# Kernel optimization log

Measured on AMD Instinct MI355X. Metric: run time of the kernel, lower is better.

Reference implementation:

```python
import jax, jax.numpy as jnp
import numpy as np

N = 1024
D_IN = 512
D = 128
E = 8192


def setup_inputs() -> dict:
    key = jax.random.key(0)
    ks = jax.random.split(key, 7)
    return {
        "inputs": jax.random.normal(ks[0], (N, D_IN), dtype=jnp.float32),
        "adj": jax.random.uniform(ks[1], (N, N), dtype=jnp.float32),
        "weight": jax.random.normal(ks[2], (D_IN, D), dtype=jnp.float32) * 0.05,
        "weight_two": jax.random.normal(ks[3], (2 * D, D), dtype=jnp.float32) * 0.05,
        "weight_three": jax.random.normal(ks[4], (2 * D, 1), dtype=jnp.float32) * 0.05,
        "train_edges": jax.random.randint(ks[5], (E, 2), 0, N, dtype=jnp.int64 if jax.config.jax_enable_x64 else jnp.int32),
        "train_false_edges": jax.random.randint(ks[6], (E, 2), 0, N, dtype=jnp.int64 if jax.config.jax_enable_x64 else jnp.int32),
    }


def reference(inputs, adj, weight, weight_two, weight_three, train_edges, train_false_edges):
    # encoder: x = X W ; z = A x   (single GCN-style layer, no bias)
    x = inputs @ weight          # (N, D)
    z = adj @ x                  # (N, D)
    n, d = z.shape

    # all-pairs features: pair (i, j) -> [z_i ; z_j]  (torch repeat/reshape semantics)
    z1 = jnp.broadcast_to(z[:, None, :], (n, n, d))   # z1[i,j] = z[i]
    z2 = jnp.broadcast_to(z[None, :, :], (n, n, d))   # z2[i,j] = z[j]

    z_pair = jax.nn.relu(jnp.concatenate([z1, z2], axis=-1))   # (N, N, 2D)
    z_pair = jnp.einsum('ijk,kl->ijl', z_pair, weight_two)     # (N, N, D)
    z_em = z1 * z2                                             # (N, N, D)

    score = jnp.einsum('ijk,kl->ijl', jnp.concatenate([z_pair, z_em], axis=-1), weight_three)
    return jax.nn.sigmoid(score[..., 0])  # (N, N)
```

## Files before the change

### kernel.cpp

```cpp
#include <hip/hip_runtime.h>
#include <math.h>

#define NN 1024
#define DIN 512
#define DD 128

static constexpr long S = (long)NN * DD;
static constexpr long XP_OFF = 0;
static constexpr long ZP_OFF = XP_OFF + 16 * S;
static constexpr long X_OFF  = ZP_OFF + 16 * S;
static constexpr long Z_OFF  = X_OFF + S;
static constexpr long U_OFF  = Z_OFF + S;
static constexpr long A_OFF  = U_OFF + 256;
static constexpr long B_OFF  = A_OFF + NN;

__global__ __launch_bounds__(256) void gemm_part(
    const float* __restrict__ A, const float* __restrict__ B,
    float* __restrict__ Cp, int K, int Kc) {
  const int t = threadIdx.x;
  const int tx = t & 31;
  const int ty = t >> 5;
  const int row0 = blockIdx.x * 32;
  const int k0 = blockIdx.y * Kc;

  float acc[4][4] = {};

  for (int k = k0; k < k0 + Kc; k += 4) {
    float bv[4][4];
#pragma unroll
    for (int kk = 0; kk < 4; ++kk) {
      const float* Brow = &B[(long)(k + kk) * DD + tx];
#pragma unroll
      for (int mc = 0; mc < 4; ++mc) bv[kk][mc] = Brow[32 * mc];
    }
#pragma unroll
    for (int mr = 0; mr < 4; ++mr) {
      const int r = row0 + ty + 8 * mr;
      const float4 av = *(const float4*)&A[(long)r * K + k];
      const float ar[4] = {av.x, av.y, av.z, av.w};
#pragma unroll
      for (int kk = 0; kk < 4; ++kk)
#pragma unroll
        for (int mc = 0; mc < 4; ++mc) acc[mr][mc] += ar[kk] * bv[kk][mc];
    }
  }

  float* Cs = Cp + (long)blockIdx.y * S;
#pragma unroll
  for (int mr = 0; mr < 4; ++mr) {
    const int r = row0 + ty + 8 * mr;
#pragma unroll
    for (int mc = 0; mc < 4; ++mc)
      Cs[(long)r * DD + tx + 32 * mc] = acc[mr][mc];
  }
}

__global__ __launch_bounds__(256) void reduce_x_u(
    const float* __restrict__ xp, float* __restrict__ x,
    const float* __restrict__ W2, const float* __restrict__ w3,
    float* __restrict__ u) {
  const long i = (long)blockIdx.x * 256 + threadIdx.x;
  float s = 0.f;
#pragma unroll
  for (int p = 0; p < 16; ++p) s += xp[p * S + i];
  x[i] = s;

  if (blockIdx.x == 0) {
    const int kq = threadIdx.x;
    float uu = 0.f;
#pragma unroll 4
    for (int l = 0; l < DD; ++l) uu += W2[(long)kq * DD + l] * w3[l];
    u[kq] = uu;
  }
}

__global__ __launch_bounds__(128) void finalize_z(
    const float* __restrict__ zp, float* __restrict__ z,
    const float* __restrict__ u, float* __restrict__ a, float* __restrict__ b) {
  __shared__ float red[2][2];
  const int i = blockIdx.x;
  const int c = threadIdx.x;
  float s = 0.f;
#pragma unroll
  for (int p = 0; p < 16; ++p) s += zp[p * S + (long)i * DD + c];
  z[(long)i * DD + c] = s;

  const float r = s > 0.f ? s : 0.f;
  float pa = r * u[c];
  float pb = r * u[DD + c];
#pragma unroll
  for (int off = 32; off > 0; off >>= 1) {
    pa += __shfl_down(pa, off);
    pb += __shfl_down(pb, off);
  }
  const int w = c >> 6;
  if ((c & 63) == 0) { red[w][0] = pa; red[w][1] = pb; }
  __syncthreads();
  if (c == 0) {
    a[i] = red[0][0] + red[1][0];
    b[i] = red[0][1] + red[1][1];
  }
}

__global__ __launch_bounds__(256) void k4_decode(
    const float* __restrict__ z, const float* __restrict__ w3,
    const float* __restrict__ a, const float* __restrict__ b,
    float* __restrict__ out) {
  __shared__ float zwl[64 * DD];
  const int t = threadIdx.x;
  const int i0 = blockIdx.y * 64;
  const int j0 = blockIdx.x * 64;

#pragma unroll
  for (int s = 0; s < 8; ++s) {
    const int q = s * 256 + t;
    const int r = q >> 5;
    const int k4 = (q & 31) << 2;
    float4 w = *(const float4*)&z[(long)(j0 + r) * DD + k4];
    const float4 cc = *(const float4*)&w3[DD + k4];
    w.x *= cc.x; w.y *= cc.y; w.z *= cc.z; w.w *= cc.w;
    *(float4*)&zwl[r * DD + (k4 ^ ((r & 7) << 2))] = w;
  }
  __syncthreads();

  const int tx = t & 15;
  const int ty = t >> 4;
  float acc[4][4] = {};
  for (int k4 = 0; k4 < DD; k4 += 4) {
    float4 ar[4], bc[4];
#pragma unroll
    for (int m = 0; m < 4; ++m)
      ar[m] = *(const float4*)&z[(long)(i0 + ty + 16 * m) * DD + k4];
#pragma unroll
    for (int m = 0; m < 4; ++m) {
      const int C = tx + 16 * m;
      bc[m] = *(const float4*)&zwl[C * DD + (k4 ^ ((C & 7) << 2))];
    }
#pragma unroll
    for (int mr = 0; mr < 4; ++mr)
#pragma unroll
      for (int mc = 0; mc < 4; ++mc)
        acc[mr][mc] += ar[mr].x * bc[mc].x + ar[mr].y * bc[mc].y +
                       ar[mr].z * bc[mc].z + ar[mr].w * bc[mc].w;
  }

#pragma unroll
  for (int mr = 0; mr < 4; ++mr) {
    const int i = i0 + ty + 16 * mr;
    const float ai = a[i];
#pragma unroll
    for (int mc = 0; mc < 4; ++mc) {
      const int j = j0 + tx + 16 * mc;
      const float sc = ai + b[j] + acc[mr][mc];
      out[(long)i * NN + j] = 1.0f / (1.0f + __expf(-sc));
    }
  }
}

extern "C" void kernel_launch(void* const* d_in, const int* in_sizes, int n_in,
                              void* d_out, int out_size, void* d_ws, size_t ws_size,
                              hipStream_t stream) {
  (void)in_sizes; (void)n_in; (void)out_size; (void)ws_size;
  const float* inputs = (const float*)d_in[0];
  const float* adj    = (const float*)d_in[1];
  const float* weight = (const float*)d_in[2];
  const float* W2     = (const float*)d_in[3];
  const float* w3     = (const float*)d_in[4];
  float* out = (float*)d_out;

  float* ws = (float*)d_ws;
  float* xp = ws + XP_OFF;
  float* zp = ws + ZP_OFF;
  float* x  = ws + X_OFF;
  float* z  = ws + Z_OFF;
  float* u  = ws + U_OFF;
  float* a  = ws + A_OFF;
  float* b  = ws + B_OFF;

  gemm_part<<<dim3(32, 16), 256, 0, stream>>>(inputs, weight, xp, DIN, DIN / 16);
  reduce_x_u<<<512, 256, 0, stream>>>(xp, x, W2, w3, u);
  gemm_part<<<dim3(32, 16), 256, 0, stream>>>(adj, x, zp, NN, NN / 16);
  finalize_z<<<1024, 128, 0, stream>>>(zp, z, u, a, b);
  k4_decode<<<dim3(16, 16), 256, 0, stream>>>(z, w3, a, b, out);
}
```

Baseline: 109.6 us.

## Fuse all stages into one cooperative kernel with grid-wide syncs

Replaces the five separate kernel launches with a single cooperative kernel of 256 blocks that runs every stage in sequence, separated by grid.sync(). The K split of both GEMMs drops from 16 to 8 so the 256-block grid covers them, and the per-stage reductions are remapped to that block count. The aim is to remove per-launch overhead and inter-kernel gaps. In exchange, each GEMM stage now runs with half as many blocks and twice the K-chunk per block, and the grid barriers carry their own cost.

```diff
diff --git a/kernel.cpp b/kernel.cpp
--- a/kernel.cpp
+++ b/kernel.cpp
@@ -1,27 +1,30 @@
 #include <hip/hip_runtime.h>
+#include <hip/hip_cooperative_groups.h>
 #include <math.h>
+
+namespace cg = cooperative_groups;
 
 #define NN 1024
 #define DIN 512
 #define DD 128
+#define NSPLIT 8
 
 static constexpr long S = (long)NN * DD;
 static constexpr long XP_OFF = 0;
-static constexpr long ZP_OFF = XP_OFF + 16 * S;
-static constexpr long X_OFF  = ZP_OFF + 16 * S;
+static constexpr long ZP_OFF = XP_OFF + NSPLIT * S;
+static constexpr long X_OFF  = ZP_OFF + NSPLIT * S;
 static constexpr long Z_OFF  = X_OFF + S;
 static constexpr long U_OFF  = Z_OFF + S;
 static constexpr long A_OFF  = U_OFF + 256;
 static constexpr long B_OFF  = A_OFF + NN;
 
-__global__ __launch_bounds__(256) void gemm_part(
+__device__ __forceinline__ void gemm_part_dev(
     const float* __restrict__ A, const float* __restrict__ B,
-    float* __restrict__ Cp, int K, int Kc) {
-  const int t = threadIdx.x;
+    float* __restrict__ Cp, int K, int Kc, int bid, int t) {
   const int tx = t & 31;
   const int ty = t >> 5;
-  const int row0 = blockIdx.x * 32;
-  const int k0 = blockIdx.y * Kc;
+  const int row0 = (bid & 31) * 32;
+  const int k0 = (bid >> 5) * Kc;
 
   float acc[4][4] = {};
 
@@ -45,7 +48,7 @@
     }
   }
 
-  float* Cs = Cp + (long)blockIdx.y * S;
+  float* Cs = Cp + (long)(bid >> 5) * S;
 #pragma unroll
   for (int mr = 0; mr < 4; ++mr) {
     const int r = row0 + ty + 8 * mr;
@@ -55,104 +58,125 @@
   }
 }
 
-__global__ __launch_bounds__(256) void reduce_x_u(
-    const float* __restrict__ xp, float* __restrict__ x,
-    const float* __restrict__ W2, const float* __restrict__ w3,
-    float* __restrict__ u) {
-  const long i = (long)blockIdx.x * 256 + threadIdx.x;
-  float s = 0.f;
-#pragma unroll
-  for (int p = 0; p < 16; ++p) s += xp[p * S + i];
-  x[i] = s;
-
-  if (blockIdx.x == 0) {
-    const int kq = threadIdx.x;
-    float uu = 0.f;
-#pragma unroll 4
-    for (int l = 0; l < DD; ++l) uu += W2[(long)kq * DD + l] * w3[l];
-    u[kq] = uu;
-  }
-}
-
-__global__ __launch_bounds__(128) void finalize_z(
-    const float* __restrict__ zp, float* __restrict__ z,
-    const float* __restrict__ u, float* __restrict__ a, float* __restrict__ b) {
-  __shared__ float red[2][2];
-  const int i = blockIdx.x;
-  const int c = threadIdx.x;
-  float s = 0.f;
-#pragma unroll
-  for (int p = 0; p < 16; ++p) s += zp[p * S + (long)i * DD + c];
-  z[(long)i * DD + c] = s;
-
-  const float r = s > 0.f ? s : 0.f;
-  float pa = r * u[c];
-  float pb = r * u[DD + c];
-#pragma unroll
-  for (int off = 32; off > 0; off >>= 1) {
-    pa += __shfl_down(pa, off);
-    pb += __shfl_down(pb, off);
-  }
-  const int w = c >> 6;
-  if ((c & 63) == 0) { red[w][0] = pa; red[w][1] = pb; }
-  __syncthreads();
-  if (c == 0) {
-    a[i] = red[0][0] + red[1][0];
-    b[i] = red[0][1] + red[1][1];
-  }
-}
-
-__global__ __launch_bounds__(256) void k4_decode(
-    const float* __restrict__ z, const float* __restrict__ w3,
-    const float* __restrict__ a, const float* __restrict__ b,
-    float* __restrict__ out) {
+__global__ __launch_bounds__(256) void fused(
+    const float* __restrict__ inputs, const float* __restrict__ adj,
+    const float* __restrict__ weight, const float* __restrict__ W2,
+    const float* __restrict__ w3, float* __restrict__ out,
+    float* __restrict__ ws) {
+  cg::grid_group grid = cg::this_grid();
   __shared__ float zwl[64 * DD];
+
   const int t = threadIdx.x;
-  const int i0 = blockIdx.y * 64;
-  const int j0 = blockIdx.x * 64;
-
-#pragma unroll
-  for (int s = 0; s < 8; ++s) {
-    const int q = s * 256 + t;
-    const int r = q >> 5;
-    const int k4 = (q & 31) << 2;
-    float4 w = *(const float4*)&z[(long)(j0 + r) * DD + k4];
-    const float4 cc = *(const float4*)&w3[DD + k4];
-    w.x *= cc.x; w.y *= cc.y; w.z *= cc.z; w.w *= cc.w;
-    *(float4*)&zwl[r * DD + (k4 ^ ((r & 7) << 2))] = w;
-  }
-  __syncthreads();
-
-  const int tx = t & 15;
-  const int ty = t >> 4;
-  float acc[4][4] = {};
-  for (int k4 = 0; k4 < DD; k4 += 4) {
-    float4 ar[4], bc[4];
-#pragma unroll
-    for (int m = 0; m < 4; ++m)
-      ar[m] = *(const float4*)&z[(long)(i0 + ty + 16 * m) * DD + k4];
-#pragma unroll
-    for (int m = 0; m < 4; ++m) {
-      const int C = tx + 16 * m;
-      bc[m] = *(const float4*)&zwl[C * DD + (k4 ^ ((C & 7) << 2))];
-    }
-#pragma unroll
-    for (int mr = 0; mr < 4; ++mr)
-#pragma unroll
-      for (int mc = 0; mc < 4; ++mc)
-        acc[mr][mc] += ar[mr].x * bc[mc].x + ar[mr].y * bc[mc].y +
-                       ar[mr].z * bc[mc].z + ar[mr].w * bc[mc].w;
-  }
-
-#pragma unroll
-  for (int mr = 0; mr < 4; ++mr) {
-    const int i = i0 + ty + 16 * mr;
-    const float ai = a[i];
-#pragma unroll
-    for (int mc = 0; mc < 4; ++mc) {
-      const int j = j0 + tx + 16 * mc;
-      const float sc = ai + b[j] + acc[mr][mc];
-      out[(long)i * NN + j] = 1.0f / (1.0f + __expf(-sc));
+  const int bid = blockIdx.x;
+
+  float* xp = ws + XP_OFF;
+  float* zp = ws + ZP_OFF;
+  float* x  = ws + X_OFF;
+  float* z  = ws + Z_OFF;
+  float* u  = ws + U_OFF;
+  float* a  = ws + A_OFF;
+  float* b  = ws + B_OFF;
+
+  gemm_part_dev(inputs, weight, xp, DIN, DIN / NSPLIT, bid, t);
+  grid.sync();
+
+  {
+    const long i0 = (long)bid * 512;
+    float s0 = 0.f, s1 = 0.f;
+#pragma unroll
+    for (int p = 0; p < NSPLIT; ++p) {
+      s0 += xp[p * S + i0 + t];
+      s1 += xp[p * S + i0 + 256 + t];
+    }
+    x[i0 + t] = s0;
+    x[i0 + 256 + t] = s1;
+
+    if (t < 64) {
+      float p = W2[(long)bid * DD + t] * w3[t] +
+                W2[(long)bid * DD + 64 + t] * w3[64 + t];
+#pragma unroll
+      for (int off = 32; off > 0; off >>= 1) p += __shfl_down(p, off);
+      if (t == 0) u[bid] = p;
+    }
+  }
+  grid.sync();
+
+  gemm_part_dev(adj, x, zp, NN, NN / NSPLIT, bid, t);
+  grid.sync();
+
+  {
+    const int w = t >> 6;
+    const int l = t & 63;
+    const int i = 4 * bid + w;
+    const long base = (long)i * DD + 2 * l;
+    float s0 = 0.f, s1 = 0.f;
+#pragma unroll
+    for (int p = 0; p < NSPLIT; ++p) {
+      const float2 v = *(const float2*)&zp[p * S + base];
+      s0 += v.x; s1 += v.y;
+    }
+    *(float2*)&z[base] = make_float2(s0, s1);
+
+    const float r0 = s0 > 0.f ? s0 : 0.f;
+    const float r1 = s1 > 0.f ? s1 : 0.f;
+    float pa = r0 * u[2 * l] + r1 * u[2 * l + 1];
+    float pb = r0 * u[DD + 2 * l] + r1 * u[DD + 2 * l + 1];
+#pragma unroll
+    for (int off = 32; off > 0; off >>= 1) {
+      pa += __shfl_down(pa, off);
+      pb += __shfl_down(pb, off);
+    }
+    if (l == 0) { a[i] = pa; b[i] = pb; }
+  }
+  grid.sync();
+
+  {
+    const int i0 = (bid >> 4) * 64;
+    const int j0 = (bid & 15) * 64;
+
+#pragma unroll
+    for (int s = 0; s < 8; ++s) {
+      const int q = s * 256 + t;
+      const int r = q >> 5;
+      const int k4 = (q & 31) << 2;
+      float4 wv = *(const float4*)&z[(long)(j0 + r) * DD + k4];
+      const float4 cc = *(const float4*)&w3[DD + k4];
+      wv.x *= cc.x; wv.y *= cc.y; wv.z *= cc.z; wv.w *= cc.w;
+      *(float4*)&zwl[r * DD + (k4 ^ ((r & 7) << 2))] = wv;
+    }
+    __syncthreads();
+
+    const int tx = t & 15;
+    const int ty = t >> 4;
+    float acc[4][4] = {};
+    for (int k4 = 0; k4 < DD; k4 += 4) {
+      float4 ar[4], bc[4];
+#pragma unroll
+      for (int m = 0; m < 4; ++m)
+        ar[m] = *(const float4*)&z[(long)(i0 + ty + 16 * m) * DD + k4];
+#pragma unroll
+      for (int m = 0; m < 4; ++m) {
+        const int C = tx + 16 * m;
+        bc[m] = *(const float4*)&zwl[C * DD + (k4 ^ ((C & 7) << 2))];
+      }
+#pragma unroll
+      for (int mr = 0; mr < 4; ++mr)
+#pragma unroll
+        for (int mc = 0; mc < 4; ++mc)
+          acc[mr][mc] += ar[mr].x * bc[mc].x + ar[mr].y * bc[mc].y +
+                         ar[mr].z * bc[mc].z + ar[mr].w * bc[mc].w;
+    }
+
+#pragma unroll
+    for (int mr = 0; mr < 4; ++mr) {
+      const int i = i0 + ty + 16 * mr;
+      const float ai = a[i];
+#pragma unroll
+      for (int mc = 0; mc < 4; ++mc) {
+        const int j = j0 + tx + 16 * mc;
+        const float sc = ai + b[j] + acc[mr][mc];
+        out[(long)i * NN + j] = 1.0f / (1.0f + __expf(-sc));
+      }
     }
   }
 }
@@ -167,19 +191,10 @@
   const float* W2     = (const float*)d_in[3];
   const float* w3     = (const float*)d_in[4];
   float* out = (float*)d_out;
-
-  float* ws = (float*)d_ws;
-  float* xp = ws + XP_OFF;
-  float* zp = ws + ZP_OFF;
-  float* x  = ws + X_OFF;
-  float* z  = ws + Z_OFF;
-  float* u  = ws + U_OFF;
-  float* a  = ws + A_OFF;
-  float* b  = ws + B_OFF;
-
-  gemm_part<<<dim3(32, 16), 256, 0, stream>>>(inputs, weight, xp, DIN, DIN / 16);
-  reduce_x_u<<<512, 256, 0, stream>>>(xp, x, W2, w3, u);
-  gemm_part<<<dim3(32, 16), 256, 0, stream>>>(adj, x, zp, NN, NN / 16);
-  finalize_z<<<1024, 128, 0, stream>>>(zp, z, u, a, b);
-  k4_decode<<<dim3(16, 16), 256, 0, stream>>>(z, w3, a, b, out);
+  float* ws  = (float*)d_ws;
+
+  void* args[] = {(void*)&inputs, (void*)&adj, (void*)&weight, (void*)&W2,
+                  (void*)&w3, (void*)&out, (void*)&ws};
+  hipLaunchCooperativeKernel((const void*)fused, dim3(256), dim3(256), args,
+                             0, stream);
 }
```

Result: slower. 236.5 us (+115.7%).

## Retile GEMMs to 16-row blocks with 8-way K split and vectorized loads

Applied to the files above, without the earlier changes.

The split-K GEMMs now use 16-row tiles with float4 loads and stores of B and C, and the K split drops from 16 to 8 partials, which shrinks the partial-sum buffers and the reduction reads. The W2·w3 vector product moves out of the reduce kernel into an extra grid row of the first GEMM, so it runs alongside that GEMM. The decode kernel uses 32-row output tiles, which doubles its block count to 512 for better CU coverage. Each thread now does less arithmetic per load, so the per-block work and reuse are lower.

```diff
diff --git a/kernel.cpp b/kernel.cpp
--- a/kernel.cpp
+++ b/kernel.cpp
@@ -4,74 +4,84 @@
 #define NN 1024
 #define DIN 512
 #define DD 128
+#define NSPLIT 8
 
 static constexpr long S = (long)NN * DD;
 static constexpr long XP_OFF = 0;
-static constexpr long ZP_OFF = XP_OFF + 16 * S;
-static constexpr long X_OFF  = ZP_OFF + 16 * S;
+static constexpr long ZP_OFF = XP_OFF + NSPLIT * S;
+static constexpr long X_OFF  = ZP_OFF + NSPLIT * S;
 static constexpr long Z_OFF  = X_OFF + S;
 static constexpr long U_OFF  = Z_OFF + S;
 static constexpr long A_OFF  = U_OFF + 256;
 static constexpr long B_OFF  = A_OFF + NN;
 
-__global__ __launch_bounds__(256) void gemm_part(
+__global__ __launch_bounds__(256) void gemm16(
     const float* __restrict__ A, const float* __restrict__ B,
-    float* __restrict__ Cp, int K, int Kc) {
+    float* __restrict__ Cp, int K, int Kc,
+    const float* __restrict__ W2, const float* __restrict__ w3,
+    float* __restrict__ u) {
+  if (blockIdx.y == NSPLIT) {
+    if (blockIdx.x == 0) {
+      const int kq = threadIdx.x;
+      const float4* Wr = (const float4*)&W2[(long)kq * DD];
+      float uu = 0.f;
+#pragma unroll 8
+      for (int l = 0; l < DD / 4; ++l) {
+        const float4 wv = Wr[l];
+        const float4 cv = ((const float4*)w3)[l];
+        uu += wv.x * cv.x + wv.y * cv.y + wv.z * cv.z + wv.w * cv.w;
+      }
+      u[kq] = uu;
+    }
+    return;
+  }
+
   const int t = threadIdx.x;
   const int tx = t & 31;
   const int ty = t >> 5;
-  const int row0 = blockIdx.x * 32;
+  const int row0 = blockIdx.x * 16;
   const int k0 = blockIdx.y * Kc;
 
-  float acc[4][4] = {};
+  float acc[2][4] = {};
 
   for (int k = k0; k < k0 + Kc; k += 4) {
-    float bv[4][4];
+    float4 bv[4];
 #pragma unroll
-    for (int kk = 0; kk < 4; ++kk) {
-      const float* Brow = &B[(long)(k + kk) * DD + tx];
+    for (int kk = 0; kk < 4; ++kk)
+      bv[kk] = *(const float4*)&B[(long)(k + kk) * DD + 4 * tx];
+    float4 av[2];
 #pragma unroll
-      for (int mc = 0; mc < 4; ++mc) bv[kk][mc] = Brow[32 * mc];
-    }
+    for (int mr = 0; mr < 2; ++mr)
+      av[mr] = *(const float4*)&A[(long)(row0 + ty + 8 * mr) * K + k];
 #pragma unroll
-    for (int mr = 0; mr < 4; ++mr) {
-      const int r = row0 + ty + 8 * mr;
-      const float4 av = *(const float4*)&A[(long)r * K + k];
-      const float ar[4] = {av.x, av.y, av.z, av.w};
+    for (int mr = 0; mr < 2; ++mr) {
+      const float ar[4] = {av[mr].x, av[mr].y, av[mr].z, av[mr].w};
 #pragma unroll
-      for (int kk = 0; kk < 4; ++kk)
-#pragma unroll
-        for (int mc = 0; mc < 4; ++mc) acc[mr][mc] += ar[kk] * bv[kk][mc];
+      for (int kk = 0; kk < 4; ++kk) {
+        acc[mr][0] += ar[kk] * bv[kk].x;
+        acc[mr][1] += ar[kk] * bv[kk].y;
+        acc[mr][2] += ar[kk] * bv[kk].z;
+        acc[mr][3] += ar[kk] * bv[kk].w;
+      }
     }
   }
 
   float* Cs = Cp + (long)blockIdx.y * S;
 #pragma unroll
-  for (int mr = 0; mr < 4; ++mr) {
+  for (int mr = 0; mr < 2; ++mr) {
     const int r = row0 + ty + 8 * mr;
-#pragma unroll
-    for (int mc = 0; mc < 4; ++mc)
-      Cs[(long)r * DD + tx + 32 * mc] = acc[mr][mc];
+    *(float4*)&Cs[(long)r * DD + 4 * tx] =
+        make_float4(acc[mr][0], acc[mr][1], acc[mr][2], acc[mr][3]);
   }
 }
 
-__global__ __launch_bounds__(256) void reduce_x_u(
-    const float* __restrict__ xp, float* __restrict__ x,
-    const float* __restrict__ W2, const float* __restrict__ w3,
-    float* __restrict__ u) {
+__global__ __launch_bounds__(256) void reduce_x(
+    const float* __restrict__ xp, float* __restrict__ x) {
   const long i = (long)blockIdx.x * 256 + threadIdx.x;
   float s = 0.f;
 #pragma unroll
-  for (int p = 0; p < 16; ++p) s += xp[p * S + i];
+  for (int p = 0; p < NSPLIT; ++p) s += xp[p * S + i];
   x[i] = s;
-
-  if (blockIdx.x == 0) {
-    const int kq = threadIdx.x;
-    float uu = 0.f;
-#pragma unroll 4
-    for (int l = 0; l < DD; ++l) uu += W2[(long)kq * DD + l] * w3[l];
-    u[kq] = uu;
-  }
 }
 
 __global__ __launch_bounds__(128) void finalize_z(
@@ -82,7 +92,7 @@
   const int c = threadIdx.x;
   float s = 0.f;
 #pragma unroll
-  for (int p = 0; p < 16; ++p) s += zp[p * S + (long)i * DD + c];
+  for (int p = 0; p < NSPLIT; ++p) s += zp[p * S + (long)i * DD + c];
   z[(long)i * DD + c] = s;
 
   const float r = s > 0.f ? s : 0.f;
@@ -108,7 +118,7 @@
     float* __restrict__ out) {
   __shared__ float zwl[64 * DD];
   const int t = threadIdx.x;
-  const int i0 = blockIdx.y * 64;
+  const int i0 = blockIdx.y * 32;
   const int j0 = blockIdx.x * 64;
 
 #pragma unroll
@@ -125,11 +135,11 @@
 
   const int tx = t & 15;
   const int ty = t >> 4;
-  float acc[4][4] = {};
+  float acc[2][4] = {};
   for (int k4 = 0; k4 < DD; k4 += 4) {
-    float4 ar[4], bc[4];
+    float4 ar[2], bc[4];
 #pragma unroll
-    for (int m = 0; m < 4; ++m)
+    for (int m = 0; m < 2; ++m)
       ar[m] = *(const float4*)&z[(long)(i0 + ty + 16 * m) * DD + k4];
 #pragma unroll
     for (int m = 0; m < 4; ++m) {
@@ -137,7 +147,7 @@
       bc[m] = *(const float4*)&zwl[C * DD + (k4 ^ ((C & 7) << 2))];
     }
 #pragma unroll
-    for (int mr = 0; mr < 4; ++mr)
+    for (int mr = 0; mr < 2; ++mr)
 #pragma unroll
       for (int mc = 0; mc < 4; ++mc)
         acc[mr][mc] += ar[mr].x * bc[mc].x + ar[mr].y * bc[mc].y +
@@ -145,7 +155,7 @@
   }
 
 #pragma unroll
-  for (int mr = 0; mr < 4; ++mr) {
+  for (int mr = 0; mr < 2; ++mr) {
     const int i = i0 + ty + 16 * mr;
     const float ai = a[i];
 #pragma unroll
@@ -177,9 +187,11 @@
   float* a  = ws + A_OFF;
   float* b  = ws + B_OFF;
 
-  gemm_part<<<dim3(32, 16), 256, 0, stream>>>(inputs, weight, xp, DIN, DIN / 16);
-  reduce_x_u<<<512, 256, 0, stream>>>(xp, x, W2, w3, u);
-  gemm_part<<<dim3(32, 16), 256, 0, stream>>>(adj, x, zp, NN, NN / 16);
+  gemm16<<<dim3(64, NSPLIT + 1), 256, 0, stream>>>(inputs, weight, xp, DIN,
+                                                   DIN / NSPLIT, W2, w3, u);
+  reduce_x<<<512, 256, 0, stream>>>(xp, x);
+  gemm16<<<dim3(64, NSPLIT), 256, 0, stream>>>(adj, x, zp, NN, NN / NSPLIT,
+                                               W2, w3, u);
   finalize_z<<<1024, 128, 0, stream>>>(zp, z, u, a, b);
-  k4_decode<<<dim3(16, 16), 256, 0, stream>>>(z, w3, a, b, out);
+  k4_decode<<<dim3(16, 32), 256, 0, stream>>>(z, w3, a, b, out);
 }
```

Result: no change. 109.3 us (-0.3%).
